# Kernel tuning notes

Measured on AMD Instinct MI355X. Metric: run time of the kernel, lower is better.

Reference implementation:

```python
import jax, jax.numpy as jnp
import numpy as np

ALPHA = 0.5
SPLIT_RATIO = 0.5
NUM_HEADS = 12
LN_EPS = 1e-6


def _layernorm(x, g, b):
    m = x.mean(-1, keepdims=True)
    v = ((x - m) ** 2).mean(-1, keepdims=True)
    return (x - m) * jax.lax.rsqrt(v + LN_EPS) * g + b


def setup_inputs() -> dict:
    key = jax.random.key(0)
    ks = jax.random.split(key, 8)
    B, N1, C, L, Hm = 16, 197, 768, 4, 3072
    s = 0.02
    return {
        "x": jax.random.normal(ks[0], (B, N1, C), jnp.float32),
        "glb_cls_attn": jax.random.uniform(ks[1], (B, N1 - 1), jnp.float32),
        "split_w": jax.random.normal(ks[2], (C, 4 * C), jnp.float32) * s,
        "split_b": jnp.zeros((4 * C,), jnp.float32),
        "ln1_g": jnp.ones((L, C), jnp.float32),
        "ln1_b": jnp.zeros((L, C), jnp.float32),
        "qkv_w": jax.random.normal(ks[3], (L, C, 3 * C), jnp.float32) * s,
        "qkv_b": jnp.zeros((L, 3 * C), jnp.float32),
        "proj_w": jax.random.normal(ks[4], (L, C, C), jnp.float32) * s,
        "proj_b": jnp.zeros((L, C), jnp.float32),
        "ln2_g": jnp.ones((L, C), jnp.float32),
        "ln2_b": jnp.zeros((L, C), jnp.float32),
        "fc1_w": jax.random.normal(ks[5], (L, C, Hm), jnp.float32) * s,
        "fc1_b": jnp.zeros((L, Hm), jnp.float32),
        "fc2_w": jax.random.normal(ks[6], (L, Hm, C), jnp.float32) * s,
        "fc2_b": jnp.zeros((L, C), jnp.float32),
    }


def reference(x, glb_cls_attn, split_w, split_b, ln1_g, ln1_b, qkv_w, qkv_b,
              proj_w, proj_b, ln2_g, ln2_b, fc1_w, fc1_b, fc2_w, fc2_b):
    B, _, C = x.shape
    H = NUM_HEADS
    D = C // H
    scale = D ** -0.5

    # --- token split based on global cls attention importance ---
    cls_tok, tokens = x[:, :1], x[:, 1:]
    order = jnp.argsort(-glb_cls_attn, axis=1)  # descending importance
    tokens = jnp.take_along_axis(tokens, order[:, :, None], axis=1)
    n = tokens.shape[1]
    split_n = int(n * SPLIT_RATIO)
    st = tokens[:, :split_n] @ split_w + split_b          # [B, split_n, 4C]
    st = st.reshape(B, split_n * 4, C)                    # each token -> 4 tokens
    x = jnp.concatenate([cls_tok, st, tokens[:, split_n:]], axis=1)
    N = x.shape[1]
    glb = jnp.zeros((B, N - 1), x.dtype)

    def block(carry, p):
        x, g = carry
        g1, b1, qw, qb, pw, pb, g2, b2, w1, bb1, w2, bb2 = p
        h = _layernorm(x, g1, b1)
        qkv = (h @ qw + qb).reshape(B, N, 3, H, D).transpose(2, 0, 3, 1, 4)
        q, k, v = qkv[0], qkv[1], qkv[2]                  # [B,H,N,D]
        attn = jax.nn.softmax(jnp.einsum('bhnd,bhmd->bhnm', q, k) * scale, axis=-1)
        cls_attn = attn[:, :, 0, 1:].mean(axis=1)         # mean over heads, row 0
        o = jnp.einsum('bhnm,bhmd->bhnd', attn, v).transpose(0, 2, 1, 3).reshape(B, N, C)
        x = x + o @ pw + pb
        h2 = _layernorm(x, g2, b2)
        x = x + jax.nn.gelu(h2 @ w1 + bb1, approximate=False) @ w2 + bb2
        g = ALPHA * g + (1.0 - ALPHA) * cls_attn
        return (x, g), None

    (x, glb), _ = jax.lax.scan(
        block, (x, glb),
        (ln1_g, ln1_b, qkv_w, qkv_b, proj_w, proj_b,
         ln2_g, ln2_b, fc1_w, fc1_b, fc2_w, fc2_b))
    return x, glb
```

## Files before the change

kernel.cpp:

```cpp
#include <hip/hip_runtime.h>
#include <math.h>

typedef unsigned short u16;
typedef short s16x8 __attribute__((ext_vector_type(8)));
typedef float f32x4 __attribute__((ext_vector_type(4)));

#define BB 16
#define N1 197
#define NTOK 196
#define SPLITN 98
#define NN 491
#define CC 768
#define H3 2304
#define HM 3072
#define NH 12
#define NL 4
#define BN (BB*NN)
#define MSPLIT (BB*SPLITN)

__device__ __forceinline__ float b2f(u16 u) {
    union { unsigned int i; float f; } x; x.i = ((unsigned int)u) << 16; return x.f;
}
__device__ __forceinline__ u16 f2b(float f) {
    union { float f; unsigned int i; } x; x.f = f;
    unsigned int i = x.i;
    return (u16)((i + 0x7fffu + ((i >> 16) & 1u)) >> 16);
}
__device__ __forceinline__ float ldx(const void* p, long long i, int isf32) {
    return isf32 ? ((const float*)p)[i] : b2f(((const u16*)p)[i]);
}

__device__ __forceinline__ void gload_lds16(const u16* g, u16* l) {
    __builtin_amdgcn_global_load_lds(
        (const __attribute__((address_space(1))) unsigned int*)g,
        (__attribute__((address_space(3))) unsigned int*)l,
        16, 0, 0);
}

__global__ void detect_k(const void* __restrict__ ln1_g, int* __restrict__ flag) {
    unsigned int w = ((const unsigned int*)ln1_g)[0];
    *flag = (w == 0x3F800000u) ? 1 : 0;
}

__global__ void zero_out_k(u16* __restrict__ out, long long n) {
    long long idx = (long long)blockIdx.x * 256 + threadIdx.x;
    if (idx < n) out[idx] = 0;
}

__global__ void zero_glb_k(float* __restrict__ glb) {
    int idx = blockIdx.x * 256 + threadIdx.x;
    if (idx < BB * (NN - 1)) glb[idx] = 0.0f;
}

__global__ void sort_k(const void* __restrict__ g, int* __restrict__ order,
                       const int* __restrict__ dflag) {
    __shared__ float v[256];
    int isf32 = *dflag;
    int b = blockIdx.x, t = threadIdx.x;
    float vv = -1e30f;
    if (t < NTOK) {
        vv = ldx(g, (long long)b * NTOK + t, isf32);
        if (!(vv == vv)) vv = -1e30f;
    }
    v[t] = vv;
    __syncthreads();
    if (t < NTOK) {
        float mv = v[t]; int r = 0;
        for (int j = 0; j < NTOK; j++) {
            float vj = v[j];
            if (vj > mv || (vj == mv && j < t)) r++;
        }
        order[b * NTOK + r] = t;
    }
}

__device__ __forceinline__ int clamp_tok(int tok) {
    return (tok < 0) ? 0 : (tok > NTOK - 1 ? NTOK - 1 : tok);
}

__global__ void gather_split_k(const void* __restrict__ x_in, const int* __restrict__ order,
                               u16* __restrict__ Asp, const int* __restrict__ dflag) {
    int isf32 = *dflag;
    long long idx = (long long)blockIdx.x * 256 + threadIdx.x;
    if (idx >= (long long)MSPLIT * CC) return;
    int c = (int)(idx % CC); int m = (int)(idx / CC); int b = m / SPLITN, r = m % SPLITN;
    int tok = clamp_tok(order[b * NTOK + r]);
    Asp[idx] = f2b(ldx(x_in, ((long long)b * N1 + 1 + tok) * CC + c, isf32));
}

__global__ void build_x_k(const void* __restrict__ x_in, const u16* __restrict__ st,
                          const int* __restrict__ order, float* __restrict__ x,
                          const int* __restrict__ dflag) {
    int isf32 = *dflag;
    long long idx = (long long)blockIdx.x * 256 + threadIdx.x;
    if (idx >= (long long)BN * CC) return;
    int c = (int)(idx % CC);
    int m = (int)(idx / CC);
    int b = m / NN, pos = m % NN;
    float v;
    if (pos == 0) {
        v = ldx(x_in, (long long)b * N1 * CC + c, isf32);
    } else if (pos < 1 + 4 * SPLITN) {
        int tt = pos - 1; int r = tt >> 2, kq = tt & 3;
        v = b2f(st[((long long)b * SPLITN + r) * HM + kq * CC + c]);
    } else {
        int j = pos - (1 + 4 * SPLITN);
        int tok = clamp_tok(order[b * NTOK + SPLITN + j]);
        v = ldx(x_in, ((long long)b * N1 + 1 + tok) * CC + c, isf32);
    }
    x[idx] = v;
}

__global__ void transpose_off_k(const void* __restrict__ in, u16* __restrict__ out, int K, int N,
                                long long off, const int* __restrict__ dflag) {
    __shared__ u16 tile[32][33];
    int isf32 = *dflag;
    int n0 = blockIdx.x * 32, k0 = blockIdx.y * 32;
    int tx = threadIdx.x, ty = threadIdx.y;
    for (int i = ty; i < 32; i += 8)
        tile[i][tx] = f2b(ldx(in, off + (long long)(k0 + i) * N + n0 + tx, isf32));
    __syncthreads();
    for (int i = ty; i < 32; i += 8) out[(long long)(n0 + i) * K + k0 + tx] = tile[tx][i];
}

__global__ __launch_bounds__(256) void ln_k(const float* __restrict__ x, const void* __restrict__ g,
                                            const void* __restrict__ bgain, u16* __restrict__ h,
                                            int goff, const int* __restrict__ dflag) {
    __shared__ float sb[8];
    int isf32 = *dflag;
    int row = blockIdx.x, t = threadIdx.x;
    const float* xr = x + (long long)row * CC;
    float v0 = xr[t], v1 = xr[t + 256], v2 = xr[t + 512];
    float s = v0 + v1 + v2;
    for (int o = 32; o > 0; o >>= 1) s += __shfl_down(s, o, 64);
    int lane = t & 63, w = t >> 6;
    if (lane == 0) sb[w] = s;
    __syncthreads();
    float mean = (sb[0] + sb[1] + sb[2] + sb[3]) * (1.0f / 768.0f);
    float d0 = v0 - mean, d1 = v1 - mean, d2 = v2 - mean;
    float q = d0 * d0 + d1 * d1 + d2 * d2;
    for (int o = 32; o > 0; o >>= 1) q += __shfl_down(q, o, 64);
    if (lane == 0) sb[4 + w] = q;
    __syncthreads();
    float var = (sb[4] + sb[5] + sb[6] + sb[7]) * (1.0f / 768.0f);
    float rs = rsqrtf(var + 1e-6f);
    long long o0 = (long long)row * CC;
    h[o0 + t]       = f2b(d0 * rs * ldx(g, goff + t, isf32)       + ldx(bgain, goff + t, isf32));
    h[o0 + t + 256] = f2b(d1 * rs * ldx(g, goff + t + 256, isf32) + ldx(bgain, goff + t + 256, isf32));
    h[o0 + t + 512] = f2b(d2 * rs * ldx(g, goff + t + 512, isf32) + ldx(bgain, goff + t + 512, isf32));
}

template<int TBM, int TBN>
__global__ __launch_bounds__(256) void gemm_t(const u16* __restrict__ A, const u16* __restrict__ BT,
                                              const void* __restrict__ bias, int boff,
                                              void* __restrict__ out,
                                              int M, int N, int K, int mode,
                                              const int* __restrict__ dflag) {
    constexpr int WM = TBM / 2, WN = TBN / 2, FM = WM / 16, FN = WN / 16;
    constexpr int AI = TBM / 64;
    constexpr int BI = TBN / 64;
    constexpr int LPS = AI + BI;
    __shared__ __align__(16) u16 As[3][TBM * 32];
    __shared__ __align__(16) u16 Bs[3][TBN * 32];
    int isf32 = *dflag;

    int gx = gridDim.x, gy = gridDim.y;
    int nwg = gx * gy;
    int bid0 = blockIdx.y * gx + blockIdx.x;
    int q = nwg >> 3, rr = nwg & 7;
    int xcd = bid0 & 7, sl = bid0 >> 3;
    int wg = (xcd < rr ? xcd * (q + 1) : rr * (q + 1) + (xcd - rr) * q) + sl;
    int by = wg % gy, bx = wg / gy;
    int m0 = bx * TBM, n0 = by * TBN;

    int t = threadIdx.x, wave = t >> 6, lane = t & 63;
    int wm = (wave >> 1) * WM, wn = (wave & 1) * WN;
    int fr = lane & 15, quad = lane >> 4;

    int srow = lane >> 2;
    int scol = ((lane & 3) ^ ((srow >> 1) & 3)) * 8;

    f32x4 acc[FM][FN];
#pragma unroll
    for (int i = 0; i < FM; i++)
#pragma unroll
        for (int j = 0; j < FN; j++) acc[i][j] = (f32x4){0.f, 0.f, 0.f, 0.f};

    const int nk = K >> 5;

    auto stage = [&](int buf, int ktile) {
        int k0 = ktile << 5;
#pragma unroll
        for (int i = 0; i < AI; i++) {
            int r0 = wave * (TBM / 4) + i * 16;
            int row = m0 + r0 + srow;
            if (row > M - 1) row = M - 1;
            gload_lds16(&A[(long long)row * K + k0 + scol], &As[buf][r0 * 32]);
        }
#pragma unroll
        for (int i = 0; i < BI; i++) {
            int r0 = wave * (TBN / 4) + i * 16;
            gload_lds16(&BT[(long long)(n0 + r0 + srow) * K + k0 + scol], &Bs[buf][r0 * 32]);
        }
    };
    auto wait_pf = [&](bool pf) {
        if (pf) {
            if constexpr (LPS == 4)      asm volatile("s_waitcnt vmcnt(4)" ::: "memory");
            else if constexpr (LPS == 3) asm volatile("s_waitcnt vmcnt(3)" ::: "memory");
            else                         asm volatile("s_waitcnt vmcnt(2)" ::: "memory");
        } else {
            asm volatile("s_waitcnt vmcnt(0)" ::: "memory");
        }
    };

    stage(0, 0);
    if (nk > 1) stage(1, 1);
    wait_pf(nk > 1);
    __builtin_amdgcn_sched_barrier(0);
    __builtin_amdgcn_s_barrier();
    __builtin_amdgcn_sched_barrier(0);

    int rofs = ((quad ^ ((fr >> 1) & 3)) * 8);
    int cur = 0, sb = 2;
    for (int kt = 0; kt < nk; kt++) {
        s16x8 af[FM], bf2[FN];
#pragma unroll
        for (int i = 0; i < FM; i++)
            af[i] = *(const s16x8*)&As[cur][(wm + i * 16 + fr) * 32 + rofs];
#pragma unroll
        for (int j = 0; j < FN; j++)
            bf2[j] = *(const s16x8*)&Bs[cur][(wn + j * 16 + fr) * 32 + rofs];
#pragma unroll
        for (int i = 0; i < FM; i++)
#pragma unroll
            for (int j = 0; j < FN; j++)
                acc[i][j] = __builtin_amdgcn_mfma_f32_16x16x32_bf16(af[i], bf2[j], acc[i][j], 0, 0, 0);
        if (kt + 1 >= nk) break;
        bool pf = (kt + 2 < nk);
        if (pf) stage(sb, kt + 2);
        wait_pf(pf);
        __builtin_amdgcn_sched_barrier(0);
        __builtin_amdgcn_s_barrier();
        __builtin_amdgcn_sched_barrier(0);
        if (++cur == 3) cur = 0;
        if (++sb == 3) sb = 0;
    }

#pragma unroll
    for (int i = 0; i < FM; i++) {
#pragma unroll
        for (int j = 0; j < FN; j++) {
#pragma unroll
            for (int r = 0; r < 4; r++) {
                int row = m0 + wm + i * 16 + quad * 4 + r;
                int col = n0 + wn + j * 16 + fr;
                if (row < M) {
                    float v = acc[i][j][r] + ldx(bias, boff + col, isf32);
                    long long idx = (long long)row * N + col;
                    if (mode == 1) ((u16*)out)[idx] = f2b(v);
                    else if (mode == 2) {
                        float gl = 0.5f * v * (1.0f + erff(v * 0.70710678118654752f));
                        ((u16*)out)[idx] = f2b(gl);
                    } else ((float*)out)[idx] += v;
                }
            }
        }
    }
}

__global__ __launch_bounds__(256, 2) void attn_mfma_k(const u16* __restrict__ qkv,
                                                      u16* __restrict__ o,
                                                      float* __restrict__ cls_partial, int b0,
                                                      int nbh) {
    int bid = blockIdx.x;
    int chunk = nbh >> 3;
    int xcd = bid & 7, s = bid >> 3;
    int qt = s & 7;
    int bh = xcd * chunk + (s >> 3);
    int lb = bh / NH, h = bh % NH;
    int i0 = qt * 64;
    int w = threadIdx.x >> 6, lane = threadIdx.x & 63;
    int fr = lane & 15, quad = lane >> 4;
    int fk = quad * 8;

    __shared__ __align__(16) u16 Qs[64][72];
    __shared__ __align__(16) u16 Ks[64][72];
    __shared__ __align__(16) u16 Vt[64][72];
    __shared__ __align__(16) u16 Pst[4][16][72];

    const long long rowbase = (long long)lb * NN * H3 + (long long)h * 64;

    {
        int t = threadIdx.x;
#pragma unroll
        for (int i = 0; i < 2; i++) {
            int e = t + i * 256;
            int r = e >> 3, c8 = (e & 7) * 8;
            uint4 v = make_uint4(0u, 0u, 0u, 0u);
            int qrow = i0 + r;
            if (qrow < NN) v = *(const uint4*)&qkv[rowbase + (long long)qrow * H3 + c8];
            *(uint4*)&Qs[r][c8] = v;
        }
    }
    __syncthreads();
    s16x8 aq0 = *(const s16x8*)&Qs[w * 16 + fr][fk];
    s16x8 aq1 = *(const s16x8*)&Qs[w * 16 + fr][32 + fk];

    f32x4 S[32];
#pragma unroll
    for (int i = 0; i < 32; i++) S[i] = (f32x4){0.f, 0.f, 0.f, 0.f};

#pragma unroll
    for (int kt = 0; kt < 8; kt++) {
        int tb = kt * 64;
        __syncthreads();
        {
            int t = threadIdx.x;
#pragma unroll
            for (int i = 0; i < 2; i++) {
                int e = t + i * 256;
                int r = e >> 3, c8 = (e & 7) * 8;
                uint4 v = make_uint4(0u, 0u, 0u, 0u);
                int krow = tb + r;
                if (krow < NN) v = *(const uint4*)&qkv[rowbase + (long long)krow * H3 + CC + c8];
                *(uint4*)&Ks[r][c8] = v;
            }
        }
        __syncthreads();
#pragma unroll
        for (int ct = 0; ct < 4; ct++) {
            s16x8 bk0 = *(const s16x8*)&Ks[ct * 16 + fr][fk];
            s16x8 bk1 = *(const s16x8*)&Ks[ct * 16 + fr][32 + fk];
            S[kt * 4 + ct] = __builtin_amdgcn_mfma_f32_16x16x32_bf16(aq0, bk0, S[kt * 4 + ct], 0, 0, 0);
            S[kt * 4 + ct] = __builtin_amdgcn_mfma_f32_16x16x32_bf16(aq1, bk1, S[kt * 4 + ct], 0, 0, 0);
        }
    }

    float mrow[4] = {-1e30f, -1e30f, -1e30f, -1e30f};
#pragma unroll
    for (int tl = 0; tl < 32; tl++) {
        int col = tl * 16 + fr;
        bool valid = col < NN;
#pragma unroll
        for (int r = 0; r < 4; r++) {
            float s2 = S[tl][r] * 0.125f;
            s2 = valid ? s2 : -1e30f;
            S[tl][r] = s2;
            mrow[r] = fmaxf(mrow[r], s2);
        }
    }
#pragma unroll
    for (int m = 1; m < 16; m <<= 1)
#pragma unroll
        for (int r = 0; r < 4; r++) mrow[r] = fmaxf(mrow[r], __shfl_xor(mrow[r], m, 64));
    float lrow[4] = {0.f, 0.f, 0.f, 0.f};
#pragma unroll
    for (int tl = 0; tl < 32; tl++)
#pragma unroll
        for (int r = 0; r < 4; r++) {
            float e = __expf(S[tl][r] - mrow[r]);
            S[tl][r] = e;
            lrow[r] += e;
        }
#pragma unroll
    for (int m = 1; m < 16; m <<= 1)
#pragma unroll
        for (int r = 0; r < 4; r++) lrow[r] += __shfl_xor(lrow[r], m, 64);
    float linv[4];
#pragma unroll
    for (int r = 0; r < 4; r++) linv[r] = 1.0f / lrow[r];

    if (qt == 0 && w == 0 && quad == 0) {
        long long cbase = (long long)((b0 + lb) * NH + h) * (NN - 1);
        float inv = linv[0];
#pragma unroll
        for (int tl = 0; tl < 32; tl++) {
            int col = tl * 16 + fr;
            if (col >= 1 && col < NN) cls_partial[cbase + col - 1] = S[tl][0] * inv;
        }
    }

    f32x4 O[4];
#pragma unroll
    for (int d = 0; d < 4; d++) O[d] = (f32x4){0.f, 0.f, 0.f, 0.f};
#pragma unroll
    for (int kt2 = 0; kt2 < 8; kt2++) {
        int vb = kt2 * 64;
        __syncthreads();
        {
            int t = threadIdx.x;
#pragma unroll
            for (int i = 0; i < 2; i++) {
                int e = t + i * 256;
                int r = e >> 3, c8 = (e & 7) * 8;
                uint4 v = make_uint4(0u, 0u, 0u, 0u);
                int vrow = vb + r;
                if (vrow < NN) v = *(const uint4*)&qkv[rowbase + (long long)vrow * H3 + 2 * CC + c8];
                union { uint4 u; u16 e8[8]; } tmp; tmp.u = v;
                int rblk = r >> 3, rin = r & 7;
#pragma unroll
                for (int j = 0; j < 8; j++) {
                    int row = c8 + j;
                    int cp = ((rblk ^ (row >> 3)) << 3) | rin;
                    Vt[row][cp] = tmp.e8[j];
                }
            }
        }
#pragma unroll
        for (int tt = 0; tt < 4; tt++) {
            int tl = kt2 * 4 + tt;
#pragma unroll
            for (int r = 0; r < 4; r++)
                Pst[w][quad * 4 + r][tt * 16 + fr] = f2b(S[tl][r]);
        }
        __syncthreads();
        s16x8 ap0 = *(const s16x8*)&Pst[w][fr][fk];
        s16x8 ap1 = *(const s16x8*)&Pst[w][fr][32 + fk];
#pragma unroll
        for (int dt = 0; dt < 4; dt++) {
            int row = dt * 16 + fr;
            int g = row >> 3;
            s16x8 bv0 = *(const s16x8*)&Vt[row][((quad ^ g) & 7) * 8];
            s16x8 bv1 = *(const s16x8*)&Vt[row][(((4 + quad) ^ g) & 7) * 8];
            O[dt] = __builtin_amdgcn_mfma_f32_16x16x32_bf16(ap0, bv0, O[dt], 0, 0, 0);
            O[dt] = __builtin_amdgcn_mfma_f32_16x16x32_bf16(ap1, bv1, O[dt], 0, 0, 0);
        }
    }

#pragma unroll
    for (int r = 0; r < 4; r++) {
        int qrow = i0 + w * 16 + quad * 4 + r;
        if (qrow < NN) {
            long long obase = ((long long)(b0 + lb) * NN + qrow) * CC + h * 64;
#pragma unroll
            for (int dt = 0; dt < 4; dt++)
                o[obase + dt * 16 + fr] = f2b(O[dt][r] * linv[r]);
        }
    }
}

__global__ void glb_update_k(const float* __restrict__ cls_partial, float* __restrict__ glb) {
    int idx = blockIdx.x * 256 + threadIdx.x;
    if (idx >= BB * (NN - 1)) return;
    int b = idx / (NN - 1), j = idx % (NN - 1);
    float s = 0;
    for (int h = 0; h < NH; h++) s += cls_partial[(long long)(b * NH + h) * (NN - 1) + j];
    glb[idx] = 0.5f * glb[idx] + 0.5f * (s / NH);
}

__global__ void finalize_k(const float* __restrict__ x, const float* __restrict__ glb,
                           void* __restrict__ out, const int* __restrict__ dflag) {
    int isf32 = *dflag;
    long long nx = (long long)BN * CC;
    long long nt = nx + (long long)BB * (NN - 1);
    long long idx = (long long)blockIdx.x * 256 + threadIdx.x;
    if (idx >= nt) return;
    float v = (idx < nx) ? x[idx] : glb[idx - nx];
    if (isf32) ((float*)out)[idx] = v;
    else ((u16*)out)[idx] = f2b(v);
}

static inline char* carve(char*& p, size_t bytes) {
    char* r = p;
    p += (bytes + 255) & ~(size_t)255;
    return r;
}
static inline size_t padb(size_t b) { return (b + 255) & ~(size_t)255; }

extern "C" void kernel_launch(void* const* d_in, const int* in_sizes, int n_in,
                              void* d_out, int out_size, void* d_ws, size_t ws_size,
                              hipStream_t stream) {
    const void* x_in    = d_in[0];
    const void* glb_in  = d_in[1];
    const void* split_w = d_in[2];
    const void* split_b = d_in[3];
    const void* ln1_g   = d_in[4];
    const void* ln1_b   = d_in[5];
    const void* qkv_w   = d_in[6];
    const void* qkv_b   = d_in[7];
    const void* proj_w  = d_in[8];
    const void* proj_b  = d_in[9];
    const void* ln2_g   = d_in[10];
    const void* ln2_b   = d_in[11];
    const void* fc1_w   = d_in[12];
    const void* fc1_b   = d_in[13];
    const void* fc2_w   = d_in[14];
    const void* fc2_b   = d_in[15];

    const size_t sz_x    = (size_t)BN * CC * 4;
    const size_t sz_h    = (size_t)BN * CC * 2;
    const size_t sz_wt   = (size_t)HM * CC * 2;
    const size_t sz_cls  = (size_t)BB * NH * (NN - 1) * 4;
    const size_t sz_glb  = (size_t)BB * (NN - 1) * 4;
    const size_t sz_ord  = (size_t)BB * NTOK * 4;

    const size_t rA2 = (size_t)BN * HM * 2;
    const size_t rA  = (size_t)BN * H3 * 2;
    const size_t rB  = (size_t)(BN / 4) * HM * 2;
    const size_t rC  = (size_t)MSPLIT * HM * 2;

    const size_t base = padb(sz_x) + padb(sz_h) + 2 * padb(sz_wt) + padb(sz_cls) +
                        padb(sz_glb) + padb(sz_ord) + 256;
    int tier; size_t rsz;
    if (ws_size >= base + padb(rA2))     { tier = 0; rsz = rA2; }
    else if (ws_size >= base + padb(rA)) { tier = 1; rsz = rA; }
    else if (ws_size >= base + padb(rB)) { tier = 2; rsz = rB; }
    else if (ws_size >= base + padb(rC)) { tier = 3; rsz = rC; }
    else {
        zero_out_k<<<(int)(((long long)out_size + 255) / 256), 256, 0, stream>>>((u16*)d_out, (long long)out_size);
        return;
    }

    char* p = (char*)d_ws;
    float* x_f32   = (float*)carve(p, sz_x);
    u16* h_buf     = (u16*)carve(p, sz_h);
    u16* region1   = (u16*)carve(p, rsz);
    u16* wtA       = (u16*)carve(p, sz_wt);
    u16* wtB       = (u16*)carve(p, sz_wt);
    float* cls_par = (float*)carve(p, sz_cls);
    float* glb_f32 = (float*)carve(p, sz_glb);
    int* order     = (int*)carve(p, sz_ord);
    int* dflag     = (int*)carve(p, 256);
    u16* Asp       = wtB;

    auto gemm = [&](const u16* A, const u16* BT, const void* bias, int boff, void* out,
                    int M, int N, int K, int mode) {
        long long b128 = (long long)((M + 127) / 128) * (N / 128);
        if ((N & 127) == 0 && b128 >= 512)
            gemm_t<128, 128><<<dim3((M + 127) / 128, N / 128), 256, 0, stream>>>(
                A, BT, bias, boff, out, M, N, K, mode, dflag);
        else if ((N & 63) == 0)
            gemm_t<128, 64><<<dim3((M + 127) / 128, N / 64), 256, 0, stream>>>(
                A, BT, bias, boff, out, M, N, K, mode, dflag);
        else
            gemm_t<64, 64><<<dim3((M + 63) / 64, N / 64), 256, 0, stream>>>(
                A, BT, bias, boff, out, M, N, K, mode, dflag);
    };

    dim3 tb(32, 8);
    detect_k<<<1, 1, 0, stream>>>(ln1_g, dflag);
    zero_glb_k<<<(BB * (NN - 1) + 255) / 256, 256, 0, stream>>>(glb_f32);
    sort_k<<<BB, 256, 0, stream>>>(glb_in, order, dflag);
    gather_split_k<<<(MSPLIT * CC + 255) / 256, 256, 0, stream>>>(x_in, order, Asp, dflag);
    transpose_off_k<<<dim3(HM / 32, CC / 32), tb, 0, stream>>>(split_w, wtA, CC, HM, 0, dflag);
    gemm(Asp, wtA, split_b, 0, region1, MSPLIT, HM, CC, 1);
    build_x_k<<<(int)(((long long)BN * CC + 255) / 256), 256, 0, stream>>>(x_in, region1, order,
                                                                           x_f32, dflag);

    const int bch  = (tier <= 1) ? BB : 4;
    const int nbch = BB / bch;
    const int matt = bch * NN;
    const int nbh  = bch * NH;
    const int nmch = (tier == 0) ? 1 : (tier == 1) ? 2 : (tier == 2) ? 4 : 8;
    const int mch  = BN / nmch;

    for (int l = 0; l < NL; l++) {
        transpose_off_k<<<dim3(H3 / 32, CC / 32), tb, 0, stream>>>(qkv_w, wtA, CC, H3,
                                                                   (long long)l * CC * H3, dflag);
        ln_k<<<BN, 256, 0, stream>>>(x_f32, ln1_g, ln1_b, h_buf, l * CC, dflag);
        for (int bc = 0; bc < nbch; bc++) {
            const u16* Ain = h_buf + (long long)bc * matt * CC;
            gemm(Ain, wtA, qkv_b, l * H3, region1, matt, H3, CC, 1);
            attn_mfma_k<<<dim3(nbh * 8), 256, 0, stream>>>(region1, h_buf, cls_par, bc * bch, nbh);
        }
        glb_update_k<<<(BB * (NN - 1) + 255) / 256, 256, 0, stream>>>(cls_par, glb_f32);
        transpose_off_k<<<dim3(CC / 32, CC / 32), tb, 0, stream>>>(proj_w, wtA, CC, CC,
                                                                   (long long)l * CC * CC, dflag);
        gemm(h_buf, wtA, proj_b, l * CC, x_f32, BN, CC, CC, 3);
        ln_k<<<BN, 256, 0, stream>>>(x_f32, ln2_g, ln2_b, h_buf, l * CC, dflag);
        transpose_off_k<<<dim3(HM / 32, CC / 32), tb, 0, stream>>>(fc1_w, wtA, CC, HM,
                                                                   (long long)l * CC * HM, dflag);
        transpose_off_k<<<dim3(CC / 32, HM / 32), tb, 0, stream>>>(fc2_w, wtB, HM, CC,
                                                                   (long long)l * HM * CC, dflag);
        for (int mc = 0; mc < nmch; mc++) {
            const u16* Ain = h_buf + (long long)mc * mch * CC;
            float* xout    = x_f32 + (long long)mc * mch * CC;
            gemm(Ain, wtA, fc1_b, l * HM, region1, mch, HM, CC, 2);
            gemm(region1, wtB, fc2_b, l * CC, xout, mch, CC, HM, 3);
        }
    }
    long long total_out = (long long)BN * CC + (long long)BB * (NN - 1);
    finalize_k<<<(int)((total_out + 255) / 256), 256, 0, stream>>>(x_f32, glb_f32, d_out, dflag);
}
```

Measured before the change: 1.664 ms.

## Unroll GEMM k-loop by triple buffer, issue prefetch before MFMA, fast GELU

The GEMM main loop is unrolled three ways so LDS buffer indices are compile-time constants. The prefetch of tile kt+2 is now issued before the MFMAs on the current tile, so global-to-LDS loads overlap compute. Per-row global offsets are also precomputed once. The GELU epilogue replaces erff with an Abramowitz-Stegun polynomial plus rcp/exp, which cuts transcendental cost but adds roughly 1e-7-scale approximation error, hidden by the bf16 output.

```diff
diff --git a/kernel.cpp b/kernel.cpp
--- a/kernel.cpp
+++ b/kernel.cpp
@@ -28,6 +28,18 @@
 }
 __device__ __forceinline__ float ldx(const void* p, long long i, int isf32) {
     return isf32 ? ((const float*)p)[i] : b2f(((const u16*)p)[i]);
+}
+
+__device__ __forceinline__ float gelu_fast(float v) {
+    float x = v * 0.70710678118654752f;
+    float ax = fabsf(x);
+    float t = __builtin_amdgcn_rcpf(fmaf(0.3275911f, ax, 1.0f));
+    float p = t * fmaf(t, fmaf(t, fmaf(t, fmaf(t, 1.061405429f, -1.453152027f),
+                                       1.421413741f), -0.284496736f), 0.254829592f);
+    float e = __expf(-ax * ax);
+    float er = fmaf(-p, e, 1.0f);
+    er = copysignf(er, x);
+    return 0.5f * v * (1.0f + er);
 }
 
 __device__ __forceinline__ void gload_lds16(const u16* g, u16* l) {
@@ -180,6 +192,21 @@
     int srow = lane >> 2;
     int scol = ((lane & 3) ^ ((srow >> 1) & 3)) * 8;
 
+    long long aoff[AI];
+    long long bofs[BI];
+#pragma unroll
+    for (int i = 0; i < AI; i++) {
+        int r0 = wave * (TBM / 4) + i * 16;
+        int row = m0 + r0 + srow;
+        if (row > M - 1) row = M - 1;
+        aoff[i] = (long long)row * K + scol;
+    }
+#pragma unroll
+    for (int i = 0; i < BI; i++) {
+        int r0 = wave * (TBN / 4) + i * 16;
+        bofs[i] = (long long)(n0 + r0 + srow) * K + scol;
+    }
+
     f32x4 acc[FM][FN];
 #pragma unroll
     for (int i = 0; i < FM; i++)
@@ -188,63 +215,60 @@
 
     const int nk = K >> 5;
 
-    auto stage = [&](int buf, int ktile) {
-        int k0 = ktile << 5;
-#pragma unroll
-        for (int i = 0; i < AI; i++) {
-            int r0 = wave * (TBM / 4) + i * 16;
-            int row = m0 + r0 + srow;
-            if (row > M - 1) row = M - 1;
-            gload_lds16(&A[(long long)row * K + k0 + scol], &As[buf][r0 * 32]);
-        }
-#pragma unroll
-        for (int i = 0; i < BI; i++) {
-            int r0 = wave * (TBN / 4) + i * 16;
-            gload_lds16(&BT[(long long)(n0 + r0 + srow) * K + k0 + scol], &Bs[buf][r0 * 32]);
-        }
-    };
-    auto wait_pf = [&](bool pf) {
-        if (pf) {
-            if constexpr (LPS == 4)      asm volatile("s_waitcnt vmcnt(4)" ::: "memory");
-            else if constexpr (LPS == 3) asm volatile("s_waitcnt vmcnt(3)" ::: "memory");
-            else                         asm volatile("s_waitcnt vmcnt(2)" ::: "memory");
-        } else {
-            asm volatile("s_waitcnt vmcnt(0)" ::: "memory");
-        }
-    };
-
-    stage(0, 0);
-    if (nk > 1) stage(1, 1);
-    wait_pf(nk > 1);
+#define STAGE(BUF, KT) do {                                                          \
+        int k0_ = (KT) << 5;                                                         \
+        _Pragma("unroll") for (int i = 0; i < AI; i++)                               \
+            gload_lds16(&A[aoff[i] + k0_], &As[BUF][(wave * (TBM / 4) + i * 16) * 32]); \
+        _Pragma("unroll") for (int i = 0; i < BI; i++)                               \
+            gload_lds16(&BT[bofs[i] + k0_], &Bs[BUF][(wave * (TBN / 4) + i * 16) * 32]); \
+    } while (0)
+
+#define WAITP(PF) do {                                                               \
+        if (PF) {                                                                    \
+            if constexpr (LPS == 4)      asm volatile("s_waitcnt vmcnt(4)" ::: "memory"); \
+            else if constexpr (LPS == 3) asm volatile("s_waitcnt vmcnt(3)" ::: "memory"); \
+            else                         asm volatile("s_waitcnt vmcnt(2)" ::: "memory"); \
+        } else                           asm volatile("s_waitcnt vmcnt(0)" ::: "memory"); \
+    } while (0)
+
+    STAGE(0, 0);
+    if (nk > 1) STAGE(1, 1);
+    WAITP(nk > 1);
     __builtin_amdgcn_sched_barrier(0);
     __builtin_amdgcn_s_barrier();
     __builtin_amdgcn_sched_barrier(0);
 
     int rofs = ((quad ^ ((fr >> 1) & 3)) * 8);
-    int cur = 0, sb = 2;
-    for (int kt = 0; kt < nk; kt++) {
-        s16x8 af[FM], bf2[FN];
-#pragma unroll
-        for (int i = 0; i < FM; i++)
-            af[i] = *(const s16x8*)&As[cur][(wm + i * 16 + fr) * 32 + rofs];
-#pragma unroll
-        for (int j = 0; j < FN; j++)
-            bf2[j] = *(const s16x8*)&Bs[cur][(wn + j * 16 + fr) * 32 + rofs];
-#pragma unroll
-        for (int i = 0; i < FM; i++)
-#pragma unroll
-            for (int j = 0; j < FN; j++)
-                acc[i][j] = __builtin_amdgcn_mfma_f32_16x16x32_bf16(af[i], bf2[j], acc[i][j], 0, 0, 0);
-        if (kt + 1 >= nk) break;
-        bool pf = (kt + 2 < nk);
-        if (pf) stage(sb, kt + 2);
-        wait_pf(pf);
-        __builtin_amdgcn_sched_barrier(0);
-        __builtin_amdgcn_s_barrier();
-        __builtin_amdgcn_sched_barrier(0);
-        if (++cur == 3) cur = 0;
-        if (++sb == 3) sb = 0;
-    }
+
+#define GSTEP(BUF, PFBUF) {                                                          \
+        bool pf_ = (kt + 2 < nk);                                                    \
+        if (pf_) STAGE(PFBUF, kt + 2);               \
+        s16x8 af_[FM], bf_[FN];                                                      \
+        _Pragma("unroll") for (int i = 0; i < FM; i++)                               \
+            af_[i] = *(const s16x8*)&As[BUF][(wm + i * 16 + fr) * 32 + rofs];        \
+        _Pragma("unroll") for (int j = 0; j < FN; j++)                               \
+            bf_[j] = *(const s16x8*)&Bs[BUF][(wn + j * 16 + fr) * 32 + rofs];        \
+        _Pragma("unroll") for (int i = 0; i < FM; i++)                               \
+            _Pragma("unroll") for (int j = 0; j < FN; j++)                           \
+                acc[i][j] = __builtin_amdgcn_mfma_f32_16x16x32_bf16(af_[i], bf_[j], acc[i][j], 0, 0, 0); \
+        if (kt + 1 < nk) {                                                           \
+            WAITP(pf_);                               \
+            __builtin_amdgcn_sched_barrier(0);                                       \
+            __builtin_amdgcn_s_barrier();                 \
+            __builtin_amdgcn_sched_barrier(0);                                       \
+        }                                                                            \
+        kt++;                                                                        \
+    }
+
+    int kt = 0;
+    while (kt < nk) {
+        GSTEP(0, 2)
+        if (kt < nk) GSTEP(1, 0)
+        if (kt < nk) GSTEP(2, 1)
+    }
+#undef GSTEP
+#undef WAITP
+#undef STAGE
 
 #pragma unroll
     for (int i = 0; i < FM; i++) {
@@ -258,10 +282,8 @@
                     float v = acc[i][j][r] + ldx(bias, boff + col, isf32);
                     long long idx = (long long)row * N + col;
                     if (mode == 1) ((u16*)out)[idx] = f2b(v);
-                    else if (mode == 2) {
-                        float gl = 0.5f * v * (1.0f + erff(v * 0.70710678118654752f));
-                        ((u16*)out)[idx] = f2b(gl);
-                    } else ((float*)out)[idx] += v;
+                    else if (mode == 2) ((u16*)out)[idx] = f2b(gelu_fast(v));
+                    else ((float*)out)[idx] += v;
                 }
             }
         }
```

Result: no change. 1.659 ms (-0.3%).
